# Kernel tuning notes

Measured on AMD Instinct MI355X. Metric: run time of the kernel, lower is better.

## Reference

```python
import jax, jax.numpy as jnp
import numpy as np

N = 50000
E = 800000
F_IN = 500
ID_DIM = 128
HID = 128
N_CLS = 40


def _init_linear(key, fan_in, fan_out, bias=True):
    k1, k2 = jax.random.split(key)
    bound = 1.0 / np.sqrt(fan_in)
    W = jax.random.uniform(k1, (fan_in, fan_out), minval=-bound, maxval=bound, dtype=jnp.float32)
    if bias:
        b = jax.random.uniform(k2, (fan_out,), minval=-bound, maxval=bound, dtype=jnp.float32)
        return W, b
    return W, None


def setup_inputs() -> dict:
    key = jax.random.key(0)
    ks = jax.random.split(key, 10)
    x = jax.random.normal(ks[0], (N, F_IN), dtype=jnp.float32)
    edge_index = jax.random.randint(ks[1], (2, E), 0, N, dtype=jnp.int32)
    W_map, b_map = _init_linear(ks[2], F_IN, ID_DIM)
    Wl1, bl1 = _init_linear(ks[3], ID_DIM, HID)
    Wr1, _ = _init_linear(ks[4], ID_DIM, HID, bias=False)
    Wl2, bl2 = _init_linear(ks[5], HID, 2 * HID)
    Wr2, _ = _init_linear(ks[6], HID, 2 * HID, bias=False)
    Wl3, bl3 = _init_linear(ks[7], 2 * HID, N_CLS)
    Wr3, _ = _init_linear(ks[8], 2 * HID, N_CLS, bias=False)
    return {"x": x, "edge_index": edge_index,
            "W_map": W_map, "b_map": b_map,
            "Wl1": Wl1, "bl1": bl1, "Wr1": Wr1,
            "Wl2": Wl2, "bl2": bl2, "Wr2": Wr2,
            "Wl3": Wl3, "bl3": bl3, "Wr3": Wr3}


def _sage_conv(x, src, dst, Wl, bl, Wr):
    # mean aggregation of source features into destination nodes
    agg = jax.ops.segment_sum(x[src], dst, num_segments=N)  # [N, d]
    cnt = jax.ops.segment_sum(jnp.ones((src.shape[0],), x.dtype), dst, num_segments=N)
    mean = agg / jnp.maximum(cnt, 1.0)[:, None]
    # SAGEConv (normalize=False): lin_l(mean_neigh) + lin_r(x), bias only on lin_l
    return mean @ Wl + bl + x @ Wr


def reference(x, edge_index, W_map, b_map, Wl1, bl1, Wr1, Wl2, bl2, Wr2, Wl3, bl3, Wr3):
    src, dst = edge_index[0], edge_index[1]
    h = x @ W_map + b_map                      # [N, 128]
    h = jax.nn.relu(_sage_conv(h, src, dst, Wl1, bl1, Wr1))   # dropout is identity in eval
    h = jax.nn.relu(_sage_conv(h, src, dst, Wl2, bl2, Wr2))
    h = _sage_conv(h, src, dst, Wl3, bl3, Wr3)
    return jax.nn.log_softmax(h, axis=1)
```

## Files before the change

### kernel.cpp

```cpp
#include <hip/hip_runtime.h>
#include <math.h>

#define NN 50000
#define NE 800000
#define FIN 500
#define NCLS 40
#define NB 196

typedef short short8 __attribute__((ext_vector_type(8)));
typedef float f32x4 __attribute__((ext_vector_type(4)));

__device__ __forceinline__ unsigned short f2bf(float f) {
    unsigned u = __float_as_uint(f);
    unsigned r = (u + 0x7FFFu + ((u >> 16) & 1u)) >> 16;
    return (unsigned short)r;
}
__device__ __forceinline__ float bf2f(unsigned short h) {
    return __uint_as_float(((unsigned)h) << 16);
}

typedef const __attribute__((address_space(1))) void gv1;
typedef __attribute__((address_space(3))) void lv3;
__device__ __forceinline__ void gl16(const void* g, void* l) {
    __builtin_amdgcn_global_load_lds((gv1*)g, (lv3*)l, 16, 0, 0);
}

__global__ void k_wsplit(const float* __restrict__ W, short* __restrict__ dst,
                         int Ksrc, int Ncols, int Kpad, int BN, int koff,
                         int noff, int llog) {
    int i = blockIdx.x * 256 + threadIdx.x;
    int len = 1 << llog;
    if (i >= Ncols * len) return;
    int n = i >> llog, kk = i & (len - 1);
    float v = (kk < Ksrc) ? W[(size_t)kk * Ncols + n] : 0.f;
    unsigned short hi = f2bf(v);
    float lo = v - bf2f(hi);
    int nd = noff + n, kd = koff + kk;
    int yb = nd / BN, r = nd % BN;
    int ck = kd >> 6, kin = kd & 63;
    int c16h = (kin >> 3) ^ (r & 7);
    size_t rowb = (((size_t)yb * (Kpad >> 6) + ck) * BN + r) * 128;
    dst[rowb + c16h * 8 + (kin & 7)] = (short)hi;
    dst[rowb + (8 + c16h) * 8 + (kin & 7)] = (short)f2bf(lo);
}

__global__ void k_count(const int* __restrict__ dst, int* __restrict__ deg) {
    int e = blockIdx.x * blockDim.x + threadIdx.x;
    if (e < NE) atomicAdd(&deg[dst[e]], 1);
}

__global__ void k_scan1(const int* __restrict__ deg, int* __restrict__ offs,
                        int* __restrict__ bsum) {
    __shared__ int sm[256];
    int tid = threadIdx.x;
    int i = blockIdx.x * 256 + tid;
    int v = (i < NN) ? deg[i] : 0;
    sm[tid] = v;
    __syncthreads();
    for (int off = 1; off < 256; off <<= 1) {
        int t = (tid >= off) ? sm[tid - off] : 0;
        __syncthreads();
        sm[tid] += t;
        __syncthreads();
    }
    if (i < NN) offs[i] = sm[tid] - v;
    if (tid == 255) bsum[blockIdx.x] = sm[255];
}

__global__ void k_scan2(const int* __restrict__ bsum, int* __restrict__ bpre,
                        int* __restrict__ offs) {
    __shared__ int sm[256];
    int tid = threadIdx.x;
    int v = (tid < NB) ? bsum[tid] : 0;
    sm[tid] = v;
    __syncthreads();
    for (int off = 1; off < 256; off <<= 1) {
        int t = (tid >= off) ? sm[tid - off] : 0;
        __syncthreads();
        sm[tid] += t;
        __syncthreads();
    }
    if (tid < NB) bpre[tid] = sm[tid] - v;
    if (tid == 255) offs[NN] = sm[255];
}

__global__ void k_scan3(int* __restrict__ offs, const int* __restrict__ bpre,
                        int* __restrict__ cursor) {
    int i = blockIdx.x * 256 + threadIdx.x;
    if (i < NN) {
        int v = offs[i] + bpre[blockIdx.x];
        offs[i] = v;
        cursor[i] = v;
    }
}

__global__ void k_scatter(const int* __restrict__ src, const int* __restrict__ dst,
                          int* __restrict__ cursor, int* __restrict__ ssrc) {
    int e = blockIdx.x * blockDim.x + threadIdx.x;
    if (e < NE) {
        int p = atomicAdd(&cursor[dst[e]], 1);
        ssrc[p] = src[e];
    }
}

__global__ __launch_bounds__(256) void k_aggb(
    const short* __restrict__ hb, const int* __restrict__ offs,
    const int* __restrict__ ssrc, short* __restrict__ mH) {
    int wid = (blockIdx.x * 256 + threadIdx.x) >> 6;
    int lane = threadIdx.x & 63;
    if (wid >= NN) return;
    int sub = lane >> 4, l16 = lane & 15;
    int beg = offs[wid], end = offs[wid + 1];
    f32x4 a0 = {0.f, 0.f, 0.f, 0.f}, a1 = {0.f, 0.f, 0.f, 0.f};
    int i = beg + sub;
    for (; i + 12 < end; i += 16) {
        int s0 = ssrc[i];
        int s1 = ssrc[i + 4];
        int s2 = ssrc[i + 8];
        int s3 = ssrc[i + 12];
        short8 v0 = *(const short8*)(hb + (size_t)s0 * 128 + l16 * 8);
        short8 v1 = *(const short8*)(hb + (size_t)s1 * 128 + l16 * 8);
        short8 v2 = *(const short8*)(hb + (size_t)s2 * 128 + l16 * 8);
        short8 v3 = *(const short8*)(hb + (size_t)s3 * 128 + l16 * 8);
#pragma unroll
        for (int j = 0; j < 4; ++j) {
            a0[j] += (bf2f((unsigned short)v0[j]) + bf2f((unsigned short)v1[j])) +
                     (bf2f((unsigned short)v2[j]) + bf2f((unsigned short)v3[j]));
            a1[j] += (bf2f((unsigned short)v0[j + 4]) + bf2f((unsigned short)v1[j + 4])) +
                     (bf2f((unsigned short)v2[j + 4]) + bf2f((unsigned short)v3[j + 4]));
        }
    }
    for (; i < end; i += 4) {
        int s0 = ssrc[i];
        short8 v0 = *(const short8*)(hb + (size_t)s0 * 128 + l16 * 8);
#pragma unroll
        for (int j = 0; j < 4; ++j) {
            a0[j] += bf2f((unsigned short)v0[j]);
            a1[j] += bf2f((unsigned short)v0[j + 4]);
        }
    }
#pragma unroll
    for (int j = 0; j < 4; ++j) {
        a0[j] += __shfl_xor(a0[j], 16);
        a0[j] += __shfl_xor(a0[j], 32);
        a1[j] += __shfl_xor(a1[j], 16);
        a1[j] += __shfl_xor(a1[j], 32);
    }
    if (sub == 0) {
        float inv = 1.f / fmaxf((float)(end - beg), 1.f);
        a0 *= inv; a1 *= inv;
        short8 hv;
#pragma unroll
        for (int j = 0; j < 4; ++j) {
            hv[j] = (short)f2bf(a0[j]);
            hv[j + 4] = (short)f2bf(a1[j]);
        }
        *(short8*)(mH + (size_t)wid * 128 + l16 * 8) = hv;
    }
}

template <int BN, int KPAD, int KS0, int KREAL, bool AFP32, bool RELU, bool PQ>
__global__ __launch_bounds__(512, 4) void k_mm8(
    const void* __restrict__ A0v, const short* __restrict__ A1,
    const short* __restrict__ Bg, const float* __restrict__ bias,
    short* __restrict__ CH, int ldc,
    float* __restrict__ F0, float* __restrict__ F1, int splitN,
    int M, int N) {
    constexpr int NT = BN / 16;
    constexpr int C = KPAD / 64;
    constexpr int PT = (BN * 16) / 512;
    constexpr int SLAB = BN * 128;
    constexpr int NA = AFP32 ? 4 : 0;
    static_assert((BN * 16) % 512 == 0, "staging divisibility");
    static_assert(C >= 3, "peel structure needs >=3 chunks");
    __shared__ short Bs[2 * SLAB];
    int tid = threadIdx.x;
    int wave = tid >> 6, lane = tid & 63;
    int quad = lane >> 4, l16 = lane & 15;
    int colBase = blockIdx.y * BN;
    int r0 = blockIdx.x * 128 + wave * 16 + l16;
    int r0c = min(r0, M - 1);
    const short* Bbase = Bg + (size_t)blockIdx.y * (C * SLAB);

    f32x4 acc[NT];
#pragma unroll
    for (int n = 0; n < NT; ++n) acc[n] = (f32x4){0.f, 0.f, 0.f, 0.f};

    auto stageB = [&](int buf, int ck) {
        const short* src = Bbase + (size_t)ck * SLAB;
        short* db = Bs + buf * SLAB;
#pragma unroll
        for (int u = 0; u < PT; ++u) {
            int base = u * 512 + wave * 64;
            gl16(src + (size_t)(base + lane) * 8, db + (size_t)base * 8);
        }
    };

    short8 aPre[AFP32 ? 2 : (2 * C)];
    short8 aCur[2];
    f32x4 fN[2][4];
    const float* Af = (const float*)A0v + (size_t)r0c * (size_t)KREAL;

    auto ldA32 = [&](int slot, int ck) {
#pragma unroll
        for (int s = 0; s < 2; ++s) {
            int kg = ck * 64 + s * 32 + quad * 8;
            f32x4 f0 = {0.f, 0.f, 0.f, 0.f}, f1 = {0.f, 0.f, 0.f, 0.f};
            if (kg < KREAL) f0 = *(const f32x4*)(Af + kg);
            if (kg + 4 < KREAL) f1 = *(const f32x4*)(Af + kg + 4);
            fN[slot][s * 2] = f0;
            fN[slot][s * 2 + 1] = f1;
        }
    };
    auto cvtA = [&](int slot) {
#pragma unroll
        for (int s = 0; s < 2; ++s) {
            short8 a;
#pragma unroll
            for (int j = 0; j < 4; ++j) {
                a[j] = (short)f2bf(fN[slot][s * 2][j]);
                a[j + 4] = (short)f2bf(fN[slot][s * 2 + 1][j]);
            }
            aCur[s] = a;
        }
    };
    auto compute = [&](int ck) {
        const short* bb = Bs + (ck & 1) * SLAB;
#pragma unroll
        for (int s = 0; s < 2; ++s) {
            short8 a;
            if constexpr (AFP32) a = aCur[s];
            else                 a = aPre[ck * 2 + s];
#pragma unroll
            for (int n = 0; n < NT; ++n) {
                int r = n * 16 + l16;
                int ch = (s * 4 + quad) ^ (r & 7);
                short8 bh = *(const short8*)(bb + r * 128 + ch * 8);
                short8 bl = *(const short8*)(bb + r * 128 + (8 + ch) * 8);
                acc[n] = __builtin_amdgcn_mfma_f32_16x16x32_bf16(a, bh, acc[n], 0, 0, 0);
                acc[n] = __builtin_amdgcn_mfma_f32_16x16x32_bf16(a, bl, acc[n], 0, 0, 0);
            }
        }
    };

    if constexpr (!AFP32) {
        const short* A0 = (const short*)A0v;
#pragma unroll
        for (int c = 0; c < C; ++c) {
            const bool seg = (c * 64 >= KS0);
            const short* ap = seg ? A1 : A0;
            const int w = seg ? (KPAD - KS0) : KS0;
            const int col = c * 64 - (seg ? KS0 : 0);
#pragma unroll
            for (int s = 0; s < 2; ++s)
                aPre[c * 2 + s] =
                    *(const short8*)(ap + (size_t)r0c * w + col + s * 32 + quad * 8);
        }
    }
    stageB(0, 0);
    if constexpr (AFP32) { ldA32(0, 0); ldA32(1, 1); }

#pragma unroll
    for (int ck = 0; ck <= C - 2; ++ck) {
        asm volatile("s_waitcnt vmcnt(%0)" ::"n"(NA) : "memory");
        __builtin_amdgcn_s_barrier();
        __builtin_amdgcn_sched_barrier(0);
        stageB((ck + 1) & 1, ck + 1);
        if constexpr (AFP32) {
            cvtA(ck & 1);
            if (ck + 2 < C) ldA32(ck & 1, ck + 2);
        }
        compute(ck);
    }
    {
        asm volatile("s_waitcnt vmcnt(0)" ::: "memory");
        __builtin_amdgcn_s_barrier();
        __builtin_amdgcn_sched_barrier(0);
        if constexpr (AFP32) cvtA((C - 1) & 1);
        compute(C - 1);
    }

    int gr0 = blockIdx.x * 128 + wave * 16 + quad * 4;
#pragma unroll
    for (int n = 0; n < NT; ++n) {
        int gc = colBase + n * 16 + l16;
        if (gc >= N) continue;
        float b = bias ? bias[gc] : 0.f;
#pragma unroll
        for (int r = 0; r < 4; ++r) {
            int gr = gr0 + r;
            if (gr < M) {
                float v = acc[n][r] + b;
                if (RELU) v = fmaxf(v, 0.f);
                if constexpr (PQ) {
                    if (gc < splitN) CH[(size_t)gr * ldc + gc] = (short)f2bf(v);
                    else             F0[(size_t)gr * (N - splitN) + (gc - splitN)] = v;
                } else {
                    if (CH) CH[(size_t)gr * ldc + gc] = (short)f2bf(v);
                    if (F0) {
                        if (gc < splitN) F0[(size_t)gr * splitN + gc] = v;
                        else             F1[(size_t)gr * (N - splitN) + (gc - splitN)] = v;
                    }
                }
            }
        }
    }
}

__global__ __launch_bounds__(256) void k_final(
    const short* __restrict__ pH, const float* __restrict__ q,
    const int* __restrict__ offs, const int* __restrict__ ssrc,
    const float* __restrict__ bl3, float* __restrict__ out) {
    int wid = (blockIdx.x * 256 + threadIdx.x) >> 6;
    int lane = threadIdx.x & 63;
    if (wid >= NN) return;
    bool act = lane < NCLS;
    int beg = offs[wid], end = offs[wid + 1];
    float a0 = 0.f, a1 = 0.f, a2 = 0.f, a3 = 0.f;
    int i = beg;
    for (; i + 3 < end; i += 4) {
        int s0 = ssrc[i], s1 = ssrc[i + 1], s2 = ssrc[i + 2], s3 = ssrc[i + 3];
        if (act) {
            a0 += bf2f((unsigned short)pH[(size_t)s0 * 64 + lane]);
            a1 += bf2f((unsigned short)pH[(size_t)s1 * 64 + lane]);
            a2 += bf2f((unsigned short)pH[(size_t)s2 * 64 + lane]);
            a3 += bf2f((unsigned short)pH[(size_t)s3 * 64 + lane]);
        }
    }
    for (; i < end; ++i) {
        int s0 = ssrc[i];
        if (act) a0 += bf2f((unsigned short)pH[(size_t)s0 * 64 + lane]);
    }
    float inv = 1.f / fmaxf((float)(end - beg), 1.f);
    float v = act ? ((a0 + a1) + (a2 + a3)) * inv + bl3[lane] + q[(size_t)wid * NCLS + lane]
                  : -INFINITY;
    float m = v;
#pragma unroll
    for (int off = 32; off > 0; off >>= 1) m = fmaxf(m, __shfl_xor(m, off));
    float e = act ? expf(v - m) : 0.f;
    float s = e;
#pragma unroll
    for (int off = 32; off > 0; off >>= 1) s += __shfl_xor(s, off);
    float ls = logf(s);
    if (act) out[(size_t)wid * NCLS + lane] = v - m - ls;
}

extern "C" void kernel_launch(void* const* d_in, const int* in_sizes, int n_in,
                              void* d_out, int out_size, void* d_ws, size_t ws_size,
                              hipStream_t stream) {
    const float* x    = (const float*)d_in[0];
    const int*   ei   = (const int*)d_in[1];
    const int*   esrc = ei;
    const int*   edst = ei + NE;
    const float* W_map = (const float*)d_in[2];
    const float* b_map = (const float*)d_in[3];
    const float* Wl1   = (const float*)d_in[4];
    const float* bl1   = (const float*)d_in[5];
    const float* Wr1   = (const float*)d_in[6];
    const float* Wl2   = (const float*)d_in[7];
    const float* bl2   = (const float*)d_in[8];
    const float* Wr2   = (const float*)d_in[9];
    const float* Wl3   = (const float*)d_in[10];
    const float* bl3   = (const float*)d_in[11];
    const float* Wr3   = (const float*)d_in[12];
    float* out = (float*)d_out;

    char* ws = (char*)d_ws;
    short* h0H = (short*)ws; ws += (size_t)NN * 128 * 2;
    short* m0H = (short*)ws; ws += (size_t)NN * 128 * 2;
    short* h1H = (short*)ws; ws += (size_t)NN * 128 * 2;
    short* m1H = (short*)ws; ws += (size_t)NN * 128 * 2;
    short* h2H = (short*)ws; ws += (size_t)NN * 256 * 2;
    short* pH  = (short*)ws; ws += (size_t)NN * 64 * 2;
    float* q   = (float*)ws; ws += (size_t)NN * NCLS * 4;
    short* wt  = (short*)ws; ws += (size_t)376832 * 2;
    int* deg    = (int*)ws;  ws += (size_t)NN * 4;
    int* offs   = (int*)ws;  ws += (size_t)(NN + 2) * 4;
    int* cursor = (int*)ws;  ws += (size_t)NN * 4;
    int* ssrc   = (int*)ws;  ws += (size_t)NE * 4;
    int* bsum   = (int*)ws;  ws += (size_t)256 * 4;
    int* bpre   = (int*)ws;  ws += (size_t)256 * 4;

    short* m_w  = wt + 0;
    short* b1w  = wt + 131072;
    short* b2w  = wt + 196608;
    short* b3w  = wt + 327680;

    (void)hipMemsetAsync(b3w, 0, (size_t)49152 * 2, stream);
    k_wsplit<<<(128 * 512 + 255) / 256, 256, 0, stream>>>(W_map, m_w, FIN, 128, 512, 128, 0, 0, 9);
    k_wsplit<<<(128 * 128 + 255) / 256, 256, 0, stream>>>(Wr1, b1w, 128, 128, 256, 128, 0, 0, 7);
    k_wsplit<<<(128 * 128 + 255) / 256, 256, 0, stream>>>(Wl1, b1w, 128, 128, 256, 128, 128, 0, 7);
    k_wsplit<<<(256 * 128 + 255) / 256, 256, 0, stream>>>(Wr2, b2w, 128, 256, 256, 128, 0, 0, 7);
    k_wsplit<<<(256 * 128 + 255) / 256, 256, 0, stream>>>(Wl2, b2w, 128, 256, 256, 128, 128, 0, 7);
    k_wsplit<<<(40 * 256 + 255) / 256, 256, 0, stream>>>(Wl3, b3w, 256, 40, 256, 96, 0, 0, 8);
    k_wsplit<<<(40 * 256 + 255) / 256, 256, 0, stream>>>(Wr3, b3w, 256, 40, 256, 96, 0, 40, 8);

    (void)hipMemsetAsync(deg, 0, (size_t)NN * 4, stream);
    k_count<<<(NE + 255) / 256, 256, 0, stream>>>(edst, deg);
    k_scan1<<<NB, 256, 0, stream>>>(deg, offs, bsum);
    k_scan2<<<1, 256, 0, stream>>>(bsum, bpre, offs);
    k_scan3<<<NB, 256, 0, stream>>>(offs, bpre, cursor);
    k_scatter<<<(NE + 255) / 256, 256, 0, stream>>>(esrc, edst, cursor, ssrc);

    const int g128 = (NN + 127) / 128;
    const int aggBlocks = (NN * 64) / 256;

    k_mm8<128, 512, 512, FIN, true, false, false><<<dim3(g128, 1), 512, 0, stream>>>(
        (const void*)x, nullptr, m_w, b_map,
        h0H, 128, nullptr, nullptr, 0, NN, 128);

    k_aggb<<<aggBlocks, 256, 0, stream>>>(h0H, offs, ssrc, m0H);

    k_mm8<128, 256, 128, 256, false, true, false><<<dim3(g128, 1), 512, 0, stream>>>(
        (const void*)h0H, m0H, b1w, bl1,
        h1H, 128, nullptr, nullptr, 0, NN, 128);

    k_aggb<<<aggBlocks, 256, 0, stream>>>(h1H, offs, ssrc, m1H);

    k_mm8<128, 256, 128, 256, false, true, false><<<dim3(g128, 2), 512, 0, stream>>>(
        (const void*)h1H, m1H, b2w, bl2,
        h2H, 256, nullptr, nullptr, 0, NN, 256);

    k_mm8<96, 256, 256, 256, false, false, true><<<dim3(g128, 1), 512, 0, stream>>>(
        (const void*)h2H, nullptr, b3w, nullptr,
        pH, 64, q, nullptr, NCLS, NN, 80);

    k_final<<<aggBlocks, 256, 0, stream>>>(pH, q, offs, ssrc, bl3, out);
}
```

Baseline: 462.1 us.

## Split-K the input projection GEMM and combine partials in a separate kernel

The x @ W_map GEMM is split into two K halves along a new grid z dimension, each writing fp32 partial results to a workspace. A new combine kernel sums the partials, adds the bias and converts to bf16. This is meant to raise block count and occupancy for the first GEMM, at the cost of extra fp32 partial traffic and an additional launch.

```diff
diff --git a/kernel.cpp b/kernel.cpp
--- a/kernel.cpp
+++ b/kernel.cpp
@@ -159,7 +159,7 @@
     }
 }
 
-template <int BN, int KPAD, int KS0, int KREAL, bool AFP32, bool RELU, bool PQ>
+template <int BN, int KPAD, int KS0, int KREAL, bool AFP32, bool RELU, bool PQ, bool PART>
 __global__ __launch_bounds__(512, 4) void k_mm8(
     const void* __restrict__ A0v, const short* __restrict__ A1,
     const short* __restrict__ Bg, const float* __restrict__ bias,
@@ -178,9 +178,10 @@
     int wave = tid >> 6, lane = tid & 63;
     int quad = lane >> 4, l16 = lane & 15;
     int colBase = blockIdx.y * BN;
+    int koff = blockIdx.z * KPAD;
     int r0 = blockIdx.x * 128 + wave * 16 + l16;
     int r0c = min(r0, M - 1);
-    const short* Bbase = Bg + (size_t)blockIdx.y * (C * SLAB);
+    const short* Bbase = Bg + ((size_t)blockIdx.y * gridDim.z + blockIdx.z) * (C * SLAB);
 
     f32x4 acc[NT];
 #pragma unroll
@@ -204,7 +205,7 @@
     auto ldA32 = [&](int slot, int ck) {
 #pragma unroll
         for (int s = 0; s < 2; ++s) {
-            int kg = ck * 64 + s * 32 + quad * 8;
+            int kg = koff + ck * 64 + s * 32 + quad * 8;
             f32x4 f0 = {0.f, 0.f, 0.f, 0.f}, f1 = {0.f, 0.f, 0.f, 0.f};
             if (kg < KREAL) f0 = *(const f32x4*)(Af + kg);
             if (kg + 4 < KREAL) f1 = *(const f32x4*)(Af + kg + 4);
@@ -285,14 +286,16 @@
     for (int n = 0; n < NT; ++n) {
         int gc = colBase + n * 16 + l16;
         if (gc >= N) continue;
-        float b = bias ? bias[gc] : 0.f;
+        float b = (!PART && bias) ? bias[gc] : 0.f;
 #pragma unroll
         for (int r = 0; r < 4; ++r) {
             int gr = gr0 + r;
             if (gr < M) {
                 float v = acc[n][r] + b;
                 if (RELU) v = fmaxf(v, 0.f);
-                if constexpr (PQ) {
+                if constexpr (PART) {
+                    F0[((size_t)blockIdx.z * M + gr) * ldc + gc] = v;
+                } else if constexpr (PQ) {
                     if (gc < splitN) CH[(size_t)gr * ldc + gc] = (short)f2bf(v);
                     else             F0[(size_t)gr * (N - splitN) + (gc - splitN)] = v;
                 } else {
@@ -305,6 +308,28 @@
             }
         }
     }
+}
+
+__global__ __launch_bounds__(256) void k_comb(
+    const float* __restrict__ P, const float* __restrict__ bias,
+    short* __restrict__ outH) {
+    int idx = blockIdx.x * 256 + threadIdx.x;
+    if (idx >= NN * 16) return;
+    size_t off = (size_t)idx * 8;
+    int col = (idx & 15) * 8;
+    f32x4 a0 = *(const f32x4*)(P + off);
+    f32x4 a1 = *(const f32x4*)(P + off + 4);
+    f32x4 b0 = *(const f32x4*)(P + (size_t)NN * 128 + off);
+    f32x4 b1 = *(const f32x4*)(P + (size_t)NN * 128 + off + 4);
+    f32x4 c0 = *(const f32x4*)(bias + col);
+    f32x4 c1 = *(const f32x4*)(bias + col + 4);
+    short8 hv;
+#pragma unroll
+    for (int j = 0; j < 4; ++j) {
+        hv[j] = (short)f2bf(a0[j] + b0[j] + c0[j]);
+        hv[j + 4] = (short)f2bf(a1[j] + b1[j] + c1[j]);
+    }
+    *(short8*)(outH + off) = hv;
 }
 
 __global__ __launch_bounds__(256) void k_final(
@@ -380,6 +405,7 @@
     int* ssrc   = (int*)ws;  ws += (size_t)NE * 4;
     int* bsum   = (int*)ws;  ws += (size_t)256 * 4;
     int* bpre   = (int*)ws;  ws += (size_t)256 * 4;
+    float* pk   = (float*)ws; ws += (size_t)2 * NN * 128 * 4;
 
     short* m_w  = wt + 0;
     short* b1w  = wt + 131072;
@@ -405,23 +431,24 @@
     const int g128 = (NN + 127) / 128;
     const int aggBlocks = (NN * 64) / 256;
 
-    k_mm8<128, 512, 512, FIN, true, false, false><<<dim3(g128, 1), 512, 0, stream>>>(
-        (const void*)x, nullptr, m_w, b_map,
-        h0H, 128, nullptr, nullptr, 0, NN, 128);
+    k_mm8<128, 256, 256, FIN, true, false, false, true><<<dim3(g128, 1, 2), 512, 0, stream>>>(
+        (const void*)x, nullptr, m_w, nullptr,
+        nullptr, 128, pk, nullptr, 0, NN, 128);
+    k_comb<<<(NN * 16 + 255) / 256, 256, 0, stream>>>(pk, b_map, h0H);
 
     k_aggb<<<aggBlocks, 256, 0, stream>>>(h0H, offs, ssrc, m0H);
 
-    k_mm8<128, 256, 128, 256, false, true, false><<<dim3(g128, 1), 512, 0, stream>>>(
+    k_mm8<128, 256, 128, 256, false, true, false, false><<<dim3(g128, 1), 512, 0, stream>>>(
         (const void*)h0H, m0H, b1w, bl1,
         h1H, 128, nullptr, nullptr, 0, NN, 128);
 
     k_aggb<<<aggBlocks, 256, 0, stream>>>(h1H, offs, ssrc, m1H);
 
-    k_mm8<128, 256, 128, 256, false, true, false><<<dim3(g128, 2), 512, 0, stream>>>(
+    k_mm8<128, 256, 128, 256, false, true, false, false><<<dim3(g128, 2), 512, 0, stream>>>(
         (const void*)h1H, m1H, b2w, bl2,
         h2H, 256, nullptr, nullptr, 0, NN, 256);
 
-    k_mm8<96, 256, 256, 256, false, false, true><<<dim3(g128, 1), 512, 0, stream>>>(
+    k_mm8<96, 256, 256, 256, false, false, true, false><<<dim3(g128, 1), 512, 0, stream>>>(
         (const void*)h2H, nullptr, b3w, nullptr,
         pH, 64, q, nullptr, NCLS, NN, 80);
 
```

Result: slower. 491.3 us (+6.3%).
